# Performance work log

Measured on AMD Instinct MI355X. Metric: run time of the kernel, lower is better.

The kernel has to match this reference:

```python
import jax, jax.numpy as jnp
import numpy as np

B = 32; H = 56; W = 56; C = 384; NH = 12; WS = 7; SS = 3
N = WS * WS            # tokens per window = 49
NW = (H // WS) * (W // WS)  # windows per image = 64
HD = C // NH           # head dim = 32
MLP_H = 4 * C
EPS = 1e-5


def _rel_pos_index():
    coords = np.stack(np.meshgrid(np.arange(WS), np.arange(WS), indexing='ij'))
    cf = coords.reshape(2, -1)                      # (2, N)
    rel = cf[:, :, None] - cf[:, None, :]           # (2, N, N)
    rel = rel.transpose(1, 2, 0).astype(np.int64)   # (N, N, 2)
    rel[..., 0] += WS - 1
    rel[..., 1] += WS - 1
    rel[..., 0] *= 2 * WS - 1
    return rel.sum(-1)                               # (N, N)


def _attn_mask():
    img = np.zeros((H, W))
    cnt = 0
    slc = (slice(0, -WS), slice(-WS, -SS), slice(-SS, None))
    for hs in slc:
        for ws in slc:
            img[hs, ws] = cnt
            cnt += 1
    mw = img.reshape(H // WS, WS, W // WS, WS).transpose(0, 2, 1, 3).reshape(-1, N)  # (NW, N)
    diff = mw[:, None, :] - mw[:, :, None]
    return np.where(diff != 0, -100.0, 0.0).astype(np.float32)  # (NW, N, N)


_RPI = jnp.asarray(_rel_pos_index())
_MASK = jnp.asarray(_attn_mask())


def _ln(x, w, b):
    m = jnp.mean(x, axis=-1, keepdims=True)
    v = jnp.mean((x - m) ** 2, axis=-1, keepdims=True)
    return (x - m) * jax.lax.rsqrt(v + EPS) * w + b


def _window_partition(x):  # (B,H,W,C) -> (B*NW, WS, WS, C)
    x = x.reshape(B, H // WS, WS, W // WS, WS, C)
    return x.transpose(0, 1, 3, 2, 4, 5).reshape(-1, WS, WS, C)


def _window_reverse(xw):  # (B*NW, WS, WS, C) -> (B,H,W,C)
    x = xw.reshape(B, H // WS, W // WS, WS, WS, C)
    return x.transpose(0, 1, 3, 2, 4, 5).reshape(B, H, W, C)


def setup_inputs() -> dict:
    key = jax.random.key(0)
    ks = jax.random.split(key, 8)
    s = 0.02
    return {
        'x': jax.random.normal(ks[0], (B, H * W, C), jnp.float32),
        'norm1_w': jnp.ones((C,), jnp.float32),
        'norm1_b': jnp.zeros((C,), jnp.float32),
        'qkv_w': jax.random.normal(ks[1], (C, 3 * C), jnp.float32) * s,
        'qkv_b': jnp.zeros((3 * C,), jnp.float32),
        'rpb_table': jax.random.normal(ks[2], ((2 * WS - 1) * (2 * WS - 1), NH), jnp.float32) * s,
        'proj_w': jax.random.normal(ks[3], (C, C), jnp.float32) * s,
        'proj_b': jnp.zeros((C,), jnp.float32),
        'norm2_w': jnp.ones((C,), jnp.float32),
        'norm2_b': jnp.zeros((C,), jnp.float32),
        'fc1_w': jax.random.normal(ks[4], (C, MLP_H), jnp.float32) * s,
        'fc1_b': jnp.zeros((MLP_H,), jnp.float32),
        'fc2_w': jax.random.normal(ks[5], (MLP_H, C), jnp.float32) * s,
        'fc2_b': jnp.zeros((C,), jnp.float32),
    }


def reference(x, norm1_w, norm1_b, qkv_w, qkv_b, rpb_table, proj_w, proj_b,
              norm2_w, norm2_b, fc1_w, fc1_b, fc2_w, fc2_b):
    shortcut = x
    xn = _ln(x, norm1_w, norm1_b).reshape(B, H, W, C)
    # cyclic shift
    xs = jnp.roll(xn, shift=(-SS, -SS), axis=(1, 2))
    xw = _window_partition(xs).reshape(-1, N, C)           # (B*NW, N, C)

    qkv = (xw @ qkv_w + qkv_b).reshape(-1, N, 3, NH, HD)
    qkv = qkv.transpose(2, 0, 3, 1, 4)                      # (3, B*NW, NH, N, HD)
    q, k, v = qkv[0], qkv[1], qkv[2]
    q = q * (HD ** -0.5)
    attn = jnp.einsum('bhnd,bhmd->bhnm', q, k)              # (B*NW, NH, N, N)

    bias = rpb_table[_RPI.reshape(-1)].reshape(N, N, NH).transpose(2, 0, 1)
    attn = attn + bias[None]
    # shift mask: (NW, N, N) broadcast over batch and heads
    attn = attn.reshape(B, NW, NH, N, N) + _MASK[None, :, None]
    attn = jax.nn.softmax(attn.reshape(-1, NH, N, N), axis=-1)

    out = jnp.einsum('bhnm,bhmd->bhnd', attn, v)            # (B*NW, NH, N, HD)
    out = out.transpose(0, 2, 1, 3).reshape(-1, N, C)
    out = out @ proj_w + proj_b

    out = _window_reverse(out.reshape(-1, WS, WS, C))
    out = jnp.roll(out, shift=(SS, SS), axis=(1, 2)).reshape(B, H * W, C)

    x = shortcut + out
    h = _ln(x, norm2_w, norm2_b)
    h = jax.nn.gelu(h @ fc1_w + fc1_b, approximate=False) @ fc2_w + fc2_b
    return x + h
```

## Files before the change

kernel.cpp:

```cpp
#include <hip/hip_runtime.h>
#include <hip/hip_bf16.h>
#include <math.h>


typedef short bf16x8 __attribute__((ext_vector_type(8)));
typedef float f32x4 __attribute__((ext_vector_type(4)));

#define GLOAD_LDS16(g, s)                                                      \
    __builtin_amdgcn_global_load_lds(                                          \
        (const __attribute__((address_space(1))) void*)(g),                    \
        (__attribute__((address_space(3))) void*)(s), 16, 0, 0)

__global__ __launch_bounds__(256) void wconv_k(const float* __restrict__ W,
                                               __hip_bfloat16* __restrict__ Wt,
                                               int K, int Nc) {
    int id = blockIdx.x * 256 + threadIdx.x;
    if (id >= K * Nc) return;
    int k = id / Nc, n = id % Nc;
    Wt[(size_t)n * K + k] = __float2bfloat16(W[id]);
}

__global__ __launch_bounds__(256) void biasm_k(const float* __restrict__ rpb,
                                               float* __restrict__ biasM) {
    int id = blockIdx.x * 256 + threadIdx.x;
    if (id >= 12 * 49 * 49) return;
    int h = id / 2401, rem = id % 2401, i = rem / 49, j = rem % 49;
    int ih = i / 7, iw = i % 7, jh = j / 7, jw = j % 7;
    int idx = (ih - jh + 6) * 13 + (iw - jw + 6);
    biasM[id] = rpb[idx * 12 + h];
}

template <int MODE>
__global__ __launch_bounds__(256) void ln_k(const float* __restrict__ X,
                                            const float* __restrict__ w,
                                            const float* __restrict__ b,
                                            __hip_bfloat16* __restrict__ out) {
    int wv = threadIdx.x >> 6, lane = threadIdx.x & 63;
    int row = blockIdx.x * 4 + wv;
    size_t src_row;
    if (MODE == 0) {
        int wi = row / 49, t = row % 49;
        int bb = wi >> 6, wrem = wi & 63;
        int wh = wrem >> 3, ww = wrem & 7;
        int th = t / 7, tw = t % 7;
        int hi = (wh * 7 + th + 3) % 56;
        int wimg = (ww * 7 + tw + 3) % 56;
        src_row = (size_t)(bb * 3136 + hi * 56 + wimg);
    } else {
        src_row = row;
    }
    const float* src = X + src_row * 384;
    float v[6];
    float s = 0.f, sq = 0.f;
#pragma unroll
    for (int i = 0; i < 6; i++) {
        v[i] = src[lane + i * 64];
        s += v[i];
        sq += v[i] * v[i];
    }
#pragma unroll
    for (int m = 32; m >= 1; m >>= 1) {
        s += __shfl_xor(s, m, 64);
        sq += __shfl_xor(sq, m, 64);
    }
    float mean = s * (1.f / 384.f);
    float var = sq * (1.f / 384.f) - mean * mean;
    float rstd = rsqrtf(var + 1e-5f);
    size_t orow = (size_t)row * 384;
#pragma unroll
    for (int i = 0; i < 6; i++) {
        int c = lane + i * 64;
        out[orow + c] = __float2bfloat16((v[i] - mean) * rstd * w[c] + b[c]);
    }
}

template <int EPI>
__global__ __launch_bounds__(256) void gemm_k(
    const __hip_bfloat16* __restrict__ A, const __hip_bfloat16* __restrict__ Bt,
    const float* __restrict__ bias, int K, int nTilesN,
    __hip_bfloat16* outb, float* outf, const float* resin) {
    __shared__ __align__(16) __hip_bfloat16 Asm[128 * 32];
    __shared__ __align__(16) __hip_bfloat16 Bsm[128 * 32];
    int bid = blockIdx.x;
    int tM = bid / nTilesN, tN = bid % nTilesN;
    size_t m0 = (size_t)tM * 128;
    int n0 = tN * 128;
    int tid = threadIdx.x, wv = tid >> 6, lane = tid & 63;
    int wr = wv >> 1, wc = wv & 1;
    int lm = lane & 15, lg = lane >> 4;

    f32x4 acc[4][4];
#pragma unroll
    for (int i = 0; i < 4; i++)
#pragma unroll
        for (int j = 0; j < 4; j++) acc[i][j] = (f32x4){0.f, 0.f, 0.f, 0.f};

    int c0 = wv * 2;
    int rA0 = c0 * 16 + (lane >> 2);
    int kk = (lane & 3) * 8;

    int nkt = K >> 5;
    for (int kt = 0; kt < nkt; kt++) {
        int k0 = kt << 5;
        GLOAD_LDS16(A + (m0 + rA0) * K + k0 + kk, &Asm[c0 * 512]);
        GLOAD_LDS16(A + (m0 + rA0 + 16) * K + k0 + kk, &Asm[(c0 + 1) * 512]);
        GLOAD_LDS16(Bt + (size_t)(n0 + rA0) * K + k0 + kk, &Bsm[c0 * 512]);
        GLOAD_LDS16(Bt + (size_t)(n0 + rA0 + 16) * K + k0 + kk, &Bsm[(c0 + 1) * 512]);
        __syncthreads();
        bf16x8 af[4], bfg[4];
#pragma unroll
        for (int i = 0; i < 4; i++)
            af[i] = *(const bf16x8*)&Asm[(wr * 64 + i * 16 + lm) * 32 + lg * 8];
#pragma unroll
        for (int j = 0; j < 4; j++)
            bfg[j] = *(const bf16x8*)&Bsm[(wc * 64 + j * 16 + lm) * 32 + lg * 8];
#pragma unroll
        for (int i = 0; i < 4; i++)
#pragma unroll
            for (int j = 0; j < 4; j++)
                acc[i][j] = __builtin_amdgcn_mfma_f32_16x16x32_bf16(
                    af[i], bfg[j], acc[i][j], 0, 0, 0);
        __syncthreads();
    }

    int ld = nTilesN * 128;
#pragma unroll
    for (int i = 0; i < 4; i++) {
#pragma unroll
        for (int r = 0; r < 4; r++) {
            int row = (int)m0 + wr * 64 + i * 16 + lg * 4 + r;
#pragma unroll
            for (int j = 0; j < 4; j++) {
                int col = n0 + wc * 64 + j * 16 + lm;
                float val = acc[i][j][r] + bias[col];
                if (EPI == 0) {
                    outb[(size_t)row * ld + col] = __float2bfloat16(val);
                } else if (EPI == 2) {
                    float g = 0.5f * val * (1.f + erff(val * 0.70710678118f));
                    outb[(size_t)row * ld + col] = __float2bfloat16(g);
                } else if (EPI == 1) {
                    int wi = row / 49, t = row % 49;
                    int bb = wi >> 6, wrem = wi & 63;
                    int wh = wrem >> 3, ww = wrem & 7;
                    int th = t / 7, tw = t % 7;
                    int hi = (wh * 7 + th + 3) % 56;
                    int wimg = (ww * 7 + tw + 3) % 56;
                    size_t pos = (size_t)(bb * 3136 + hi * 56 + wimg) * 384 + col;
                    outf[pos] = resin[pos] + val;
                } else {
                    size_t pos = (size_t)row * 384 + col;
                    outf[pos] = resin[pos] + val;
                }
            }
        }
    }
}

__global__ __launch_bounds__(256) void attn_k(const __hip_bfloat16* __restrict__ qkv,
                                              const float* __restrict__ biasM,
                                              __hip_bfloat16* __restrict__ out) {
    __shared__ __align__(16) __hip_bfloat16 vt[32 * 64];
    __shared__ __align__(16) __hip_bfloat16 P[64 * 64];
    int bid = blockIdx.x;
    int wi = bid / 12, h = bid % 12;
    int tid = threadIdx.x, wv = tid >> 6, lane = tid & 63;
    int lm = lane & 15, lg = lane >> 4;
    int wrem = wi & 63, wh = wrem >> 3, ww = wrem & 7;

#pragma unroll
    for (int i = 0; i < 8; i++) vt[tid * 8 + i] = __float2bfloat16(0.f);
    __syncthreads();
    if (tid < 196) {
        int t = tid >> 2, d0 = (tid & 3) * 8;
        bf16x8 vv = *(const bf16x8*)(qkv + (size_t)(wi * 49 + t) * 1152 + 768 + h * 32 + d0);
#pragma unroll
        for (int i = 0; i < 8; i++) vt[(d0 + i) * 64 + t] = ((__hip_bfloat16*)&vv)[i];
    }

    int qrow = wv * 16 + lm;
    if (qrow > 48) qrow = 48;
    bf16x8 aq = *(const bf16x8*)(qkv + (size_t)(wi * 49 + qrow) * 1152 + h * 32 + lg * 8);
    f32x4 S[4];
#pragma unroll
    for (int ct = 0; ct < 4; ct++) {
        int krow = ct * 16 + lm;
        if (krow > 48) krow = 48;
        bf16x8 bk = *(const bf16x8*)(qkv + (size_t)(wi * 49 + krow) * 1152 + 384 + h * 32 + lg * 8);
        S[ct] = __builtin_amdgcn_mfma_f32_16x16x32_bf16(aq, bk, (f32x4){0.f, 0.f, 0.f, 0.f}, 0, 0, 0);
    }

    const float scale = 0.17677669529663687f;
#pragma unroll
    for (int r = 0; r < 4; r++) {
        int irow = wv * 16 + lg * 4 + r;
        int ic = irow <= 48 ? irow : 48;
        int ith = ic / 7, itw = ic % 7;
        int ihs = wh * 7 + ith, iws = ww * 7 + itw;
        int ridi = (ihs < 49 ? 0 : (ihs < 53 ? 1 : 2)) * 3 + (iws < 49 ? 0 : (iws < 53 ? 1 : 2));
        float vals[4];
        float mx = -1e30f;
#pragma unroll
        for (int ct = 0; ct < 4; ct++) {
            int jcol = ct * 16 + lm;
            float sv;
            if (jcol < 49) {
                int jth = jcol / 7, jtw = jcol % 7;
                int jhs = wh * 7 + jth, jws = ww * 7 + jtw;
                int ridj = (jhs < 49 ? 0 : (jhs < 53 ? 1 : 2)) * 3 + (jws < 49 ? 0 : (jws < 53 ? 1 : 2));
                sv = S[ct][r] * scale + biasM[h * 2401 + ic * 49 + jcol] +
                     (ridi != ridj ? -100.f : 0.f);
            } else {
                sv = -1e30f;
            }
            vals[ct] = sv;
            mx = fmaxf(mx, sv);
        }
#pragma unroll
        for (int m = 8; m >= 1; m >>= 1) mx = fmaxf(mx, __shfl_xor(mx, m, 64));
        float sum = 0.f;
#pragma unroll
        for (int ct = 0; ct < 4; ct++) {
            vals[ct] = __expf(vals[ct] - mx);
            sum += vals[ct];
        }
#pragma unroll
        for (int m = 8; m >= 1; m >>= 1) sum += __shfl_xor(sum, m, 64);
        float inv = 1.f / sum;
#pragma unroll
        for (int ct = 0; ct < 4; ct++)
            P[irow * 64 + ct * 16 + lm] = __float2bfloat16(vals[ct] * inv);
    }
    __syncthreads();

    f32x4 O[2] = {{0.f, 0.f, 0.f, 0.f}, {0.f, 0.f, 0.f, 0.f}};
#pragma unroll
    for (int ks = 0; ks < 2; ks++) {
        bf16x8 ap = *(const bf16x8*)&P[(wv * 16 + lm) * 64 + ks * 32 + lg * 8];
#pragma unroll
        for (int nt = 0; nt < 2; nt++) {
            bf16x8 bv = *(const bf16x8*)&vt[(nt * 16 + lm) * 64 + ks * 32 + lg * 8];
            O[nt] = __builtin_amdgcn_mfma_f32_16x16x32_bf16(ap, bv, O[nt], 0, 0, 0);
        }
    }
#pragma unroll
    for (int r = 0; r < 4; r++) {
        int row = wv * 16 + lg * 4 + r;
        if (row < 49) {
            size_t base = (size_t)(wi * 49 + row) * 384 + h * 32;
            out[base + lm] = __float2bfloat16(O[0][r]);
            out[base + 16 + lm] = __float2bfloat16(O[1][r]);
        }
    }
}

extern "C" void kernel_launch(void* const* d_in, const int* in_sizes, int n_in,
                              void* d_out, int out_size, void* d_ws, size_t ws_size,
                              hipStream_t stream) {
    (void)in_sizes; (void)n_in; (void)out_size; (void)ws_size;
    const float* x     = (const float*)d_in[0];
    const float* n1w   = (const float*)d_in[1];
    const float* n1b   = (const float*)d_in[2];
    const float* qkvw  = (const float*)d_in[3];
    const float* qkvb  = (const float*)d_in[4];
    const float* rpb   = (const float*)d_in[5];
    const float* projw = (const float*)d_in[6];
    const float* projb = (const float*)d_in[7];
    const float* n2w   = (const float*)d_in[8];
    const float* n2b   = (const float*)d_in[9];
    const float* fc1w  = (const float*)d_in[10];
    const float* fc1b  = (const float*)d_in[11];
    const float* fc2w  = (const float*)d_in[12];
    const float* fc2b  = (const float*)d_in[13];
    float* out = (float*)d_out;

    char* ws = (char*)d_ws;
    __hip_bfloat16* wt_qkv  = (__hip_bfloat16*)(ws + 0);
    __hip_bfloat16* wt_proj = (__hip_bfloat16*)(ws + 884736);
    __hip_bfloat16* wt_fc1  = (__hip_bfloat16*)(ws + 1179648);
    __hip_bfloat16* wt_fc2  = (__hip_bfloat16*)(ws + 2359296);
    float*          biasM   = (float*)(ws + 3538944);
    __hip_bfloat16* xw      = (__hip_bfloat16*)(ws + 3654656);
    __hip_bfloat16* qkv     = (__hip_bfloat16*)(ws + 80724992);
    __hip_bfloat16* attn_o  = (__hip_bfloat16*)(ws + 311936000);
    __hip_bfloat16* hidden  = xw;
    __hip_bfloat16* hn      = attn_o;

    wconv_k<<<(384 * 1152 + 255) / 256, 256, 0, stream>>>(qkvw, wt_qkv, 384, 1152);
    wconv_k<<<(384 * 384 + 255) / 256, 256, 0, stream>>>(projw, wt_proj, 384, 384);
    wconv_k<<<(384 * 1536 + 255) / 256, 256, 0, stream>>>(fc1w, wt_fc1, 384, 1536);
    wconv_k<<<(1536 * 384 + 255) / 256, 256, 0, stream>>>(fc2w, wt_fc2, 1536, 384);
    biasm_k<<<(12 * 49 * 49 + 255) / 256, 256, 0, stream>>>(rpb, biasM);

    ln_k<0><<<25088, 256, 0, stream>>>(x, n1w, n1b, xw);
    gemm_k<0><<<784 * 9, 256, 0, stream>>>(xw, wt_qkv, qkvb, 384, 9, qkv, nullptr, nullptr);
    attn_k<<<2048 * 12, 256, 0, stream>>>(qkv, biasM, attn_o);
    gemm_k<1><<<784 * 3, 256, 0, stream>>>(attn_o, wt_proj, projb, 384, 3, nullptr, out, x);
    ln_k<1><<<25088, 256, 0, stream>>>(out, n2w, n2b, hn);
    gemm_k<2><<<784 * 12, 256, 0, stream>>>(hn, wt_fc1, fc1b, 384, 12, hidden, nullptr, nullptr);
    gemm_k<3><<<784 * 3, 256, 0, stream>>>(hidden, wt_fc2, fc2b, 1536, 3, nullptr, out, out);
}
```

Measured before the change: 1.366 ms.

## Double-buffer GEMM shared-memory tiles and merge weight prep kernels

The GEMM kernel now uses two LDS buffers per operand, prefetching the next K-tile with global_load_lds while MFMAs run on the current one, and drops the trailing barrier. This aims to overlap global memory latency with compute in all four GEMMs. The four weight-conversion launches and the bias-matrix launch are merged into one prep kernel to cut launch overhead. The prefetch is issued right after the single barrier, with no explicit wait on the async LDS loads before the next iteration's reads, so correctness depends on the barrier also draining them. LDS use per block doubles, which could lower occupancy.

```diff
diff --git a/kernel.cpp b/kernel.cpp
--- a/kernel.cpp
+++ b/kernel.cpp
@@ -11,23 +11,44 @@
         (const __attribute__((address_space(1))) void*)(g),                    \
         (__attribute__((address_space(3))) void*)(s), 16, 0, 0)
 
-__global__ __launch_bounds__(256) void wconv_k(const float* __restrict__ W,
-                                               __hip_bfloat16* __restrict__ Wt,
-                                               int K, int Nc) {
+__global__ __launch_bounds__(256) void prep_k(
+    const float* __restrict__ qkvw, const float* __restrict__ projw,
+    const float* __restrict__ fc1w, const float* __restrict__ fc2w,
+    const float* __restrict__ rpb,
+    __hip_bfloat16* __restrict__ wt_qkv, __hip_bfloat16* __restrict__ wt_proj,
+    __hip_bfloat16* __restrict__ wt_fc1, __hip_bfloat16* __restrict__ wt_fc2,
+    float* __restrict__ biasM) {
     int id = blockIdx.x * 256 + threadIdx.x;
-    if (id >= K * Nc) return;
-    int k = id / Nc, n = id % Nc;
-    Wt[(size_t)n * K + k] = __float2bfloat16(W[id]);
-}
-
-__global__ __launch_bounds__(256) void biasm_k(const float* __restrict__ rpb,
-                                               float* __restrict__ biasM) {
-    int id = blockIdx.x * 256 + threadIdx.x;
-    if (id >= 12 * 49 * 49) return;
-    int h = id / 2401, rem = id % 2401, i = rem / 49, j = rem % 49;
-    int ih = i / 7, iw = i % 7, jh = j / 7, jw = j % 7;
-    int idx = (ih - jh + 6) * 13 + (iw - jw + 6);
-    biasM[id] = rpb[idx * 12 + h];
+    if (id < 442368) {
+        int k = id / 1152, n = id % 1152;
+        wt_qkv[(size_t)n * 384 + k] = __float2bfloat16(qkvw[id]);
+        return;
+    }
+    id -= 442368;
+    if (id < 147456) {
+        int k = id / 384, n = id % 384;
+        wt_proj[(size_t)n * 384 + k] = __float2bfloat16(projw[id]);
+        return;
+    }
+    id -= 147456;
+    if (id < 589824) {
+        int k = id / 1536, n = id % 1536;
+        wt_fc1[(size_t)n * 384 + k] = __float2bfloat16(fc1w[id]);
+        return;
+    }
+    id -= 589824;
+    if (id < 589824) {
+        int k = id / 384, n = id % 384;
+        wt_fc2[(size_t)n * 1536 + k] = __float2bfloat16(fc2w[id]);
+        return;
+    }
+    id -= 589824;
+    if (id < 28812) {
+        int h = id / 2401, rem = id % 2401, i = rem / 49, j = rem % 49;
+        int ih = i / 7, iw = i % 7, jh = j / 7, jw = j % 7;
+        int idx = (ih - jh + 6) * 13 + (iw - jw + 6);
+        biasM[id] = rpb[idx * 12 + h];
+    }
 }
 
 template <int MODE>
@@ -79,8 +100,8 @@
     const __hip_bfloat16* __restrict__ A, const __hip_bfloat16* __restrict__ Bt,
     const float* __restrict__ bias, int K, int nTilesN,
     __hip_bfloat16* outb, float* outf, const float* resin) {
-    __shared__ __align__(16) __hip_bfloat16 Asm[128 * 32];
-    __shared__ __align__(16) __hip_bfloat16 Bsm[128 * 32];
+    __shared__ __align__(16) __hip_bfloat16 Asm[2][128 * 32];
+    __shared__ __align__(16) __hip_bfloat16 Bsm[2][128 * 32];
     int bid = blockIdx.x;
     int tM = bid / nTilesN, tN = bid % nTilesN;
     size_t m0 = (size_t)tM * 128;
@@ -98,29 +119,39 @@
     int c0 = wv * 2;
     int rA0 = c0 * 16 + (lane >> 2);
     int kk = (lane & 3) * 8;
+    const __hip_bfloat16* Ap = A + (m0 + rA0) * K + kk;
+    const __hip_bfloat16* Bp = Bt + (size_t)(n0 + rA0) * K + kk;
 
     int nkt = K >> 5;
+    {
+        GLOAD_LDS16(Ap, &Asm[0][c0 * 512]);
+        GLOAD_LDS16(Ap + (size_t)16 * K, &Asm[0][(c0 + 1) * 512]);
+        GLOAD_LDS16(Bp, &Bsm[0][c0 * 512]);
+        GLOAD_LDS16(Bp + (size_t)16 * K, &Bsm[0][(c0 + 1) * 512]);
+    }
     for (int kt = 0; kt < nkt; kt++) {
-        int k0 = kt << 5;
-        GLOAD_LDS16(A + (m0 + rA0) * K + k0 + kk, &Asm[c0 * 512]);
-        GLOAD_LDS16(A + (m0 + rA0 + 16) * K + k0 + kk, &Asm[(c0 + 1) * 512]);
-        GLOAD_LDS16(Bt + (size_t)(n0 + rA0) * K + k0 + kk, &Bsm[c0 * 512]);
-        GLOAD_LDS16(Bt + (size_t)(n0 + rA0 + 16) * K + k0 + kk, &Bsm[(c0 + 1) * 512]);
+        int cur = kt & 1;
         __syncthreads();
+        if (kt + 1 < nkt) {
+            int k0 = (kt + 1) << 5;
+            GLOAD_LDS16(Ap + k0, &Asm[cur ^ 1][c0 * 512]);
+            GLOAD_LDS16(Ap + (size_t)16 * K + k0, &Asm[cur ^ 1][(c0 + 1) * 512]);
+            GLOAD_LDS16(Bp + k0, &Bsm[cur ^ 1][c0 * 512]);
+            GLOAD_LDS16(Bp + (size_t)16 * K + k0, &Bsm[cur ^ 1][(c0 + 1) * 512]);
+        }
         bf16x8 af[4], bfg[4];
 #pragma unroll
         for (int i = 0; i < 4; i++)
-            af[i] = *(const bf16x8*)&Asm[(wr * 64 + i * 16 + lm) * 32 + lg * 8];
+            af[i] = *(const bf16x8*)&Asm[cur][(wr * 64 + i * 16 + lm) * 32 + lg * 8];
 #pragma unroll
         for (int j = 0; j < 4; j++)
-            bfg[j] = *(const bf16x8*)&Bsm[(wc * 64 + j * 16 + lm) * 32 + lg * 8];
+            bfg[j] = *(const bf16x8*)&Bsm[cur][(wc * 64 + j * 16 + lm) * 32 + lg * 8];
 #pragma unroll
         for (int i = 0; i < 4; i++)
 #pragma unroll
             for (int j = 0; j < 4; j++)
                 acc[i][j] = __builtin_amdgcn_mfma_f32_16x16x32_bf16(
                     af[i], bfg[j], acc[i][j], 0, 0, 0);
-        __syncthreads();
     }
 
     int ld = nTilesN * 128;
@@ -285,11 +316,8 @@
     __hip_bfloat16* hidden  = xw;
     __hip_bfloat16* hn      = attn_o;
 
-    wconv_k<<<(384 * 1152 + 255) / 256, 256, 0, stream>>>(qkvw, wt_qkv, 384, 1152);
-    wconv_k<<<(384 * 384 + 255) / 256, 256, 0, stream>>>(projw, wt_proj, 384, 384);
-    wconv_k<<<(384 * 1536 + 255) / 256, 256, 0, stream>>>(fc1w, wt_fc1, 384, 1536);
-    wconv_k<<<(1536 * 384 + 255) / 256, 256, 0, stream>>>(fc2w, wt_fc2, 1536, 384);
-    biasm_k<<<(12 * 49 * 49 + 255) / 256, 256, 0, stream>>>(rpb, biasM);
+    prep_k<<<7025, 256, 0, stream>>>(qkvw, projw, fc1w, fc2w, rpb,
+                                     wt_qkv, wt_proj, wt_fc1, wt_fc2, biasM);
 
     ln_k<0><<<25088, 256, 0, stream>>>(x, n1w, n1b, xw);
     gemm_k<0><<<784 * 9, 256, 0, stream>>>(xw, wt_qkv, qkvb, 384, 9, qkv, nullptr, nullptr);
```

Measured after the change: 1.329 ms. 2.7% less time.
